# Optimization experiments

Hardware: AMD Instinct MI355X
Metric: run time of the kernel (lower is better)

Reference implementation:

```python
import jax, jax.numpy as jnp
import numpy as np

# Scalars from init_kwargs (qat_training=False inference path)
IN_ZP = 0
OUT_ZP = 0
IN_SCALE = 0.02
OUT_SCALE = 0.05
STRIDE = (1, 1)
PAD = (1, 1)      # (ph, pw); module pads (pw, pw, ph, ph) via F.pad
DIL = (1, 1)
GROUPS = 1
QMIN, QMAX = -128, 127  # get_quantized_range(8)


def setup_inputs() -> dict:
    key = jax.random.key(0)
    k1, k2, k3, k4 = jax.random.split(key, 4)
    x = jax.random.randint(k1, (32, 128, 56, 56), -128, 128, dtype=jnp.int32).astype(jnp.int8)
    weight = jax.random.randint(k2, (256, 128, 3, 3), -128, 128, dtype=jnp.int32).astype(jnp.int8)
    bias = jax.random.randint(k3, (256,), -1000, 1000, dtype=jnp.int32)
    weight_scale = jax.random.uniform(k4, (256,), minval=1e-3, maxval=1e-2, dtype=jnp.float32)
    return {"x": x, "weight": weight, "bias": bias, "weight_scale": weight_scale}


def reference(x, weight, bias, weight_scale):
    # Pad spatial dims with the input zero point (matches F.pad(..., value=input_zero_point))
    xp = jnp.pad(x.astype(jnp.int32),
                 ((0, 0), (0, 0), (PAD[0], PAD[0]), (PAD[1], PAD[1])),
                 constant_values=IN_ZP)
    # Exact int32-accumulate convolution (torch CPU path)
    acc = jax.lax.conv_general_dilated(
        xp, weight.astype(jnp.int32),
        window_strides=STRIDE, padding='VALID', rhs_dilation=DIL,
        dimension_numbers=('NCHW', 'OIHW', 'NCHW'),
        feature_group_count=GROUPS, preferred_element_type=jnp.int32)
    acc = acc + bias[None, :, None, None]
    # Per-output-channel requantization
    scale = (IN_SCALE * weight_scale / OUT_SCALE)[None, :, None, None]
    out = acc.astype(jnp.float32) * scale + OUT_ZP
    out = jnp.clip(jnp.round(out), QMIN, QMAX).astype(jnp.int8)
    return out
```

## Files before the change

### kernel.cpp

```cpp
#include <hip/hip_runtime.h>
#include <hip/hip_bf16.h>
#include <stdint.h>


#define NB   32
#define CIN  128
#define HO   56
#define WO   56
#define KOUT 256
#define HP   58
#define ROWB (HP * CIN)

typedef int v4i  __attribute__((ext_vector_type(4)));
typedef int v16i __attribute__((ext_vector_type(16)));

static __device__ __forceinline__ void gload_lds16(const int8_t* g, int8_t* l) {
  __builtin_amdgcn_global_load_lds(
      (const __attribute__((address_space(1))) void*)g,
      (__attribute__((address_space(3))) void*)l, 16, 0, 0);
}

__global__ __launch_bounds__(256) void pack_x_kernel(const int* __restrict__ x,
                                                     int8_t* __restrict__ xp) {
  __shared__ int t32[128][57];
  const int tid = threadIdx.x;
  const int r = blockIdx.x;
  const int n = blockIdx.y;
  const bool interior = (r >= 1) && (r <= HO);

  if (interior) {
    const int h = r - 1;
    const int* xrow = x + ((size_t)(n * CIN) * HO + h) * WO;
    #pragma unroll
    for (int it = 0; it < 7; ++it) {
      const int j = it * 256 + tid;
      const int c = j / 14;
      const int w4 = j - c * 14;
      const int4 v = *reinterpret_cast<const int4*>(xrow + c * 3136 + w4 * 4);
      t32[c][w4 * 4 + 0] = v.x;
      t32[c][w4 * 4 + 1] = v.y;
      t32[c][w4 * 4 + 2] = v.z;
      t32[c][w4 * 4 + 3] = v.w;
    }
  }
  __syncthreads();
  #pragma unroll
  for (int it = 0; it < 8; ++it) {
    const int i = it * 256 + tid;
    if (i < HP * 32) {
      const int w = i >> 5;
      const int c4 = i & 31;
      int vv = 0;
      if (interior && w >= 1 && w <= WO) {
        const int b0 = t32[c4 * 4 + 0][w - 1] & 0xff;
        const int b1 = t32[c4 * 4 + 1][w - 1] & 0xff;
        const int b2 = t32[c4 * 4 + 2][w - 1] & 0xff;
        const int b3 = t32[c4 * 4 + 3][w - 1];
        vv = b0 | (b1 << 8) | (b2 << 16) | (b3 << 24);
      }
      *reinterpret_cast<int*>(xp + ((size_t)(n * HP + r) * HP + w) * CIN + c4 * 4) = vv;
    }
  }
}

__global__ __launch_bounds__(256) void pack_w_kernel(const int* __restrict__ wgt,
                                                     int8_t* __restrict__ wq) {
  const int wid = blockIdx.x * 256 + threadIdx.x;
  const int wi = wid & 3;
  const int ci = wid >> 2;
  const int ktb = ci / 9216;
  const int r  = ci - ktb * 9216;
  const int tap = r >> 10;
  const int r2  = r & 1023;
  const int cc  = r2 >> 7;
  const int ch  = r2 & 127;
  const int k_global = ktb * 128 + ch;
  const int cin0 = cc * 16 + wi * 4;
  const int base = (k_global * CIN + cin0) * 9 + tap;
  const int v0 = wgt[base];
  const int v1 = wgt[base + 9];
  const int v2 = wgt[base + 18];
  const int v3 = wgt[base + 27];
  reinterpret_cast<int*>(wq)[wid] =
      (v0 & 0xff) | ((v1 & 0xff) << 8) | ((v2 & 0xff) << 16) | (v3 << 24);
}

__global__ __launch_bounds__(512, 4) void conv_kernel(const int8_t* __restrict__ xp,
                                                      const int8_t* __restrict__ wq,
                                                      const int* __restrict__ bias,
                                                      const float* __restrict__ wscale,
                                                      int* __restrict__ out) {
  __shared__ __align__(16) int8_t lw[2][8 * 128 * 16];
  __shared__ __align__(16) int8_t lx[(6 * HP + 8) * 8 * 16];
  __shared__ int   bsh[128];
  __shared__ float ssh[128];

  const int tid = threadIdx.x;
  const int rg = blockIdx.x;
  const int n_img = blockIdx.y;
  const int ktb = blockIdx.z;
  const int h0 = rg * 4;

  const int lane = tid & 63;
  const int wid = tid >> 6;
  const int wr = wid & 3;
  const int wh = wid >> 2;
  const int p0 = lane & 31;
  const int half = lane >> 5;

  const int8_t* xg = xp + ((size_t)(n_img * HP) + h0) * ROWB;
  const int8_t* wqt = wq + (size_t)ktb * (9 * 16384);

  #pragma unroll
  for (int it = 0; it < 6; ++it) {
    const int i = it * 512 + tid;
    if (i < 6 * HP * 8) {
      const int pf = i >> 3;
      const int cc = (i & 7) ^ (pf & 7);
      gload_lds16(xg + pf * CIN + (cc << 4), lx + i * 16);
    }
  }
  gload_lds16(wqt + tid * 16, lw[0] + tid * 16);
  gload_lds16(wqt + (512 + tid) * 16, lw[0] + (512 + tid) * 16);
  if (tid < 128) {
    const int ch = ktb * 128 + tid;
    bsh[tid] = bias[ch];
    ssh[tid] = (0.02f * wscale[ch]) / 0.05f;
  }
  __syncthreads();

  v16i acc[2][2];
  #pragma unroll
  for (int mt = 0; mt < 2; ++mt)
    #pragma unroll
    for (int nt = 0; nt < 2; ++nt)
      #pragma unroll
      for (int e = 0; e < 16; ++e) acc[mt][nt][e] = 0;

  const int chb = wh * 64;

  #pragma unroll
  for (int tap = 0; tap < 9; ++tap) {
    if (tap < 8) {
      const int8_t* wsrc = wqt + (tap + 1) * 16384;
      int8_t* ldst = lw[(tap + 1) & 1];
      gload_lds16(wsrc + tid * 16, ldst + tid * 16);
      gload_lds16(wsrc + (512 + tid) * 16, ldst + (512 + tid) * 16);
    }
    const int kh = (tap >= 3) + (tap >= 6);
    const int kw = tap - 3 * kh;
    const int8_t* lwt = lw[tap & 1];
    const int pfb = (wr + kh) * HP + kw;
    #pragma unroll
    for (int ks = 0; ks < 4; ++ks) {
      const int cch = 2 * ks + half;
      const v4i a0 = *reinterpret_cast<const v4i*>(lwt + cch * 2048 + (chb + p0) * 16);
      const v4i a1 = *reinterpret_cast<const v4i*>(lwt + cch * 2048 + (chb + 32 + p0) * 16);
      const int pf0 = pfb + p0;
      const int pf1 = pfb + 32 + p0;
      const v4i b0 = *reinterpret_cast<const v4i*>(lx + pf0 * CIN + ((cch ^ (pf0 & 7)) << 4));
      const v4i b1 = *reinterpret_cast<const v4i*>(lx + pf1 * CIN + ((cch ^ (pf1 & 7)) << 4));
      __builtin_amdgcn_s_setprio(1);
      acc[0][0] = __builtin_amdgcn_mfma_i32_32x32x32_i8(a0, b0, acc[0][0], 0, 0, 0);
      acc[1][0] = __builtin_amdgcn_mfma_i32_32x32x32_i8(a1, b0, acc[1][0], 0, 0, 0);
      acc[0][1] = __builtin_amdgcn_mfma_i32_32x32x32_i8(a0, b1, acc[0][1], 0, 0, 0);
      acc[1][1] = __builtin_amdgcn_mfma_i32_32x32x32_i8(a1, b1, acc[1][1], 0, 0, 0);
      __builtin_amdgcn_s_setprio(0);
    }
    __syncthreads();
  }

  const int h = h0 + wr;
  #pragma unroll
  for (int mt = 0; mt < 2; ++mt) {
    #pragma unroll
    for (int r = 0; r < 16; ++r) {
      const int cl = chb + mt * 32 + (r & 3) + 8 * (r >> 2) + 4 * half;
      const int bi = bsh[cl];
      const float sc = ssh[cl];
      int* ob = out + (((size_t)(n_img * KOUT + ktb * 128 + cl)) * HO + h) * WO;
      #pragma unroll
      for (int nt = 0; nt < 2; ++nt) {
        const int w = nt * 32 + p0;
        if (w < WO) {
          float v = (float)(acc[mt][nt][r] + bi) * sc;
          v = rintf(v);
          v = fminf(fmaxf(v, -128.0f), 127.0f);
          ob[w] = (int)v;
        }
      }
    }
  }
}

extern "C" void kernel_launch(void* const* d_in, const int* in_sizes, int n_in,
                              void* d_out, int out_size, void* d_ws, size_t ws_size,
                              hipStream_t stream) {
  const int* x = (const int*)d_in[0];
  const int* wgt = (const int*)d_in[1];
  const int* bias = (const int*)d_in[2];
  const float* wscale = (const float*)d_in[3];
  int* out = (int*)d_out;

  int8_t* xp = (int8_t*)d_ws;
  int8_t* wq = (int8_t*)d_ws + (size_t)NB * HP * ROWB;

  pack_x_kernel<<<dim3(HP, NB), 256, 0, stream>>>(x, xp);
  pack_w_kernel<<<288, 256, 0, stream>>>(wgt, wq);
  conv_kernel<<<dim3(14, 32, 2), 512, 0, stream>>>(xp, wq, bias, wscale, out);
}
```

Before: 182.9 us.

## Fuse input packing into conv kernel, reading int32 NCHW directly into LDS

Removes the separate pack_x kernel and its padded NHWC int8 intermediate buffer. Each conv block now reads the int32 NCHW input directly, packs 16 channels into int8 vectors in registers, applies zero padding by bounds checks and writes swizzled rows to LDS. This drops one launch and a global write-then-read of the packed tensor. In exchange each x element is read once per kt block and per overlapping row group, with strided per-channel scalar loads that coalesce poorly and run synchronously rather than as async global-to-LDS copies.

```diff
diff --git a/kernel.cpp b/kernel.cpp
--- a/kernel.cpp
+++ b/kernel.cpp
@@ -9,7 +9,6 @@
 #define WO   56
 #define KOUT 256
 #define HP   58
-#define ROWB (HP * CIN)
 
 typedef int v4i  __attribute__((ext_vector_type(4)));
 typedef int v16i __attribute__((ext_vector_type(16)));
@@ -18,49 +17,6 @@
   __builtin_amdgcn_global_load_lds(
       (const __attribute__((address_space(1))) void*)g,
       (__attribute__((address_space(3))) void*)l, 16, 0, 0);
-}
-
-__global__ __launch_bounds__(256) void pack_x_kernel(const int* __restrict__ x,
-                                                     int8_t* __restrict__ xp) {
-  __shared__ int t32[128][57];
-  const int tid = threadIdx.x;
-  const int r = blockIdx.x;
-  const int n = blockIdx.y;
-  const bool interior = (r >= 1) && (r <= HO);
-
-  if (interior) {
-    const int h = r - 1;
-    const int* xrow = x + ((size_t)(n * CIN) * HO + h) * WO;
-    #pragma unroll
-    for (int it = 0; it < 7; ++it) {
-      const int j = it * 256 + tid;
-      const int c = j / 14;
-      const int w4 = j - c * 14;
-      const int4 v = *reinterpret_cast<const int4*>(xrow + c * 3136 + w4 * 4);
-      t32[c][w4 * 4 + 0] = v.x;
-      t32[c][w4 * 4 + 1] = v.y;
-      t32[c][w4 * 4 + 2] = v.z;
-      t32[c][w4 * 4 + 3] = v.w;
-    }
-  }
-  __syncthreads();
-  #pragma unroll
-  for (int it = 0; it < 8; ++it) {
-    const int i = it * 256 + tid;
-    if (i < HP * 32) {
-      const int w = i >> 5;
-      const int c4 = i & 31;
-      int vv = 0;
-      if (interior && w >= 1 && w <= WO) {
-        const int b0 = t32[c4 * 4 + 0][w - 1] & 0xff;
-        const int b1 = t32[c4 * 4 + 1][w - 1] & 0xff;
-        const int b2 = t32[c4 * 4 + 2][w - 1] & 0xff;
-        const int b3 = t32[c4 * 4 + 3][w - 1];
-        vv = b0 | (b1 << 8) | (b2 << 16) | (b3 << 24);
-      }
-      *reinterpret_cast<int*>(xp + ((size_t)(n * HP + r) * HP + w) * CIN + c4 * 4) = vv;
-    }
-  }
 }
 
 __global__ __launch_bounds__(256) void pack_w_kernel(const int* __restrict__ wgt,
@@ -85,7 +41,7 @@
       (v0 & 0xff) | ((v1 & 0xff) << 8) | ((v2 & 0xff) << 16) | (v3 << 24);
 }
 
-__global__ __launch_bounds__(512, 4) void conv_kernel(const int8_t* __restrict__ xp,
+__global__ __launch_bounds__(512, 4) void conv_kernel(const int* __restrict__ x,
                                                       const int8_t* __restrict__ wq,
                                                       const int* __restrict__ bias,
                                                       const float* __restrict__ wscale,
@@ -102,25 +58,40 @@
   const int h0 = rg * 4;
 
   const int lane = tid & 63;
-  const int wid = tid >> 6;
-  const int wr = wid & 3;
-  const int wh = wid >> 2;
+  const int wvi = tid >> 6;
+  const int wr = wvi & 3;
+  const int wh = wvi >> 2;
   const int p0 = lane & 31;
   const int half = lane >> 5;
 
-  const int8_t* xg = xp + ((size_t)(n_img * HP) + h0) * ROWB;
+  const int* x32 = x + (size_t)n_img * CIN * (HO * WO);
   const int8_t* wqt = wq + (size_t)ktb * (9 * 16384);
 
   #pragma unroll
   for (int it = 0; it < 6; ++it) {
     const int i = it * 512 + tid;
-    if (i < 6 * HP * 8) {
-      const int pf = i >> 3;
-      const int cc = (i & 7) ^ (pf & 7);
-      gload_lds16(xg + pf * CIN + (cc << 4), lx + i * 16);
+    if (i < 2784) {
+      const int cc = i / 348;
+      const int pf = i - cc * 348;
+      const int lr = pf / 58;
+      const int w  = pf - lr * 58;
+      const int h  = h0 + lr - 1;
+      const int wp = w - 1;
+      v4i v = {0, 0, 0, 0};
+      if ((unsigned)h < (unsigned)HO && (unsigned)wp < (unsigned)WO) {
+        const int* src = x32 + (cc * 16) * (HO * WO) + h * WO + wp;
+        int b[16];
+        #pragma unroll
+        for (int q = 0; q < 16; ++q) b[q] = src[q * (HO * WO)];
+        v[0] = (b[0] & 0xff) | ((b[1] & 0xff) << 8) | ((b[2] & 0xff) << 16) | (b[3] << 24);
+        v[1] = (b[4] & 0xff) | ((b[5] & 0xff) << 8) | ((b[6] & 0xff) << 16) | (b[7] << 24);
+        v[2] = (b[8] & 0xff) | ((b[9] & 0xff) << 8) | ((b[10] & 0xff) << 16) | (b[11] << 24);
+        v[3] = (b[12] & 0xff) | ((b[13] & 0xff) << 8) | ((b[14] & 0xff) << 16) | (b[15] << 24);
+      }
+      *reinterpret_cast<v4i*>(lx + pf * CIN + ((cc ^ (pf & 7)) << 4)) = v;
     }
   }
-  gload_lds16(wqt + tid * 16, lw[0] + tid * 16);
+  gload_lds16(wqt + tid * 16,         lw[0] + tid * 16);
   gload_lds16(wqt + (512 + tid) * 16, lw[0] + (512 + tid) * 16);
   if (tid < 128) {
     const int ch = ktb * 128 + tid;
@@ -144,7 +115,7 @@
     if (tap < 8) {
       const int8_t* wsrc = wqt + (tap + 1) * 16384;
       int8_t* ldst = lw[(tap + 1) & 1];
-      gload_lds16(wsrc + tid * 16, ldst + tid * 16);
+      gload_lds16(wsrc + tid * 16,         ldst + tid * 16);
       gload_lds16(wsrc + (512 + tid) * 16, ldst + (512 + tid) * 16);
     }
     const int kh = (tap >= 3) + (tap >= 6);
@@ -202,10 +173,8 @@
   const float* wscale = (const float*)d_in[3];
   int* out = (int*)d_out;
 
-  int8_t* xp = (int8_t*)d_ws;
-  int8_t* wq = (int8_t*)d_ws + (size_t)NB * HP * ROWB;
+  int8_t* wq = (int8_t*)d_ws;
 
-  pack_x_kernel<<<dim3(HP, NB), 256, 0, stream>>>(x, xp);
   pack_w_kernel<<<288, 256, 0, stream>>>(wgt, wq);
-  conv_kernel<<<dim3(14, 32, 2), 512, 0, stream>>>(xp, wq, bias, wscale, out);
+  conv_kernel<<<dim3(14, 32, 2), 512, 0, stream>>>(x, wq, bias, wscale, out);
 }
```

Result: no change. 184.9 us (+1.1%).
